# Performance work log

Measured on AMD Instinct MI355X. Metric: run time of the kernel, lower is better.

The kernel has to match this reference:

```python
import jax, jax.numpy as jnp
import numpy as np

B, D_IN, H = 32768, 256, 128
N_TASK, N_EXP, N_SHARE = 2, 4, 4


def setup_inputs() -> dict:
    key = jax.random.key(0)
    ks = jax.random.split(key, 4)
    s = 1.0 / np.sqrt(D_IN)
    return {
        "x": jax.random.normal(ks[0], (B, D_IN), dtype=jnp.float32),
        "W_share": jax.random.normal(ks[1], (N_SHARE, D_IN, H), dtype=jnp.float32) * s,
        "b_share": jnp.zeros((N_SHARE, H), dtype=jnp.float32),
        "W_task": jax.random.normal(ks[2], (N_TASK, N_EXP, D_IN, H), dtype=jnp.float32) * s,
        "b_task": jnp.zeros((N_TASK, N_EXP, H), dtype=jnp.float32),
        "W_gate": jax.random.normal(ks[3], (N_TASK, D_IN, N_SHARE + N_EXP), dtype=jnp.float32) * s,
        "b_gate": jnp.zeros((N_TASK, N_SHARE + N_EXP), dtype=jnp.float32),
    }


def reference(x, W_share, b_share, W_task, b_task, W_gate, b_gate):
    # shared experts: [B, N_SHARE, H]
    share = jax.nn.relu(jnp.einsum('bd,edh->beh', x, W_share) + b_share)
    # task-specific experts: [T, B, N_EXP, H]
    task = jax.nn.relu(jnp.einsum('bd,tedh->tbeh', x, W_task) + b_task[:, None])
    # gates: [T, B, N_SHARE + N_EXP], softmax over experts
    gate = jax.nn.softmax(jnp.einsum('bd,tdg->tbg', x, W_gate) + b_gate[:, None], axis=-1)
    # concat order matches original: share_net first, then task experts
    share_b = jnp.broadcast_to(share[None], (N_TASK, B, N_SHARE, H))
    experts = jnp.concatenate([share_b, task], axis=2)  # [T, B, N_SHARE+N_EXP, H]
    towers = jnp.einsum('tbeh,tbe->tbh', experts, gate)  # [T, B, H]
    return towers
```

## Files before the change

kernel.cpp:

```cpp
#include <hip/hip_runtime.h>


#define ROWSTRIDE 264
#define EXPERT_USHORTS (128 * ROWSTRIDE)
#define EXPERT_BYTES   (EXPERT_USHORTS * 2)
#define WAVE_SHARE     8448
#define WTG_USHORTS    (16 * ROWSTRIDE)

typedef __attribute__((ext_vector_type(8))) short short8;
typedef __attribute__((ext_vector_type(4))) float float4v;

__device__ __forceinline__ unsigned short f2bf(float f) {
  unsigned u = __builtin_bit_cast(unsigned, f);
  u += 0x7FFFu + ((u >> 16) & 1u);
  return (unsigned short)(u >> 16);
}

typedef const __attribute__((address_space(1))) unsigned int gu32;
typedef __attribute__((address_space(3))) unsigned int lu32;

__device__ __forceinline__ void gl_lds16(const void* g, void* l) {
  __builtin_amdgcn_global_load_lds((gu32*)g, (lu32*)l, 16, 0, 0);
}
__device__ __forceinline__ void gl_lds4(const void* g, void* l) {
  __builtin_amdgcn_global_load_lds((gu32*)g, (lu32*)l, 4, 0, 0);
}

__device__ __forceinline__ void stage_expert(const unsigned short* WT, int e,
                                             unsigned short* dst, int w, int lane) {
  const char* g = (const char*)WT + (size_t)e * EXPERT_BYTES + w * WAVE_SHARE;
  char* l = (char*)dst + w * WAVE_SHARE;
  #pragma unroll
  for (int i = 0; i < 8; ++i)
    gl_lds16(g + i * 1024 + lane * 16, l + i * 1024);
  gl_lds4(g + 8192 + lane * 4, l + 8192);
}

__global__ __launch_bounds__(256)
void prep_kernel(const float* __restrict__ Ws,
                 const float* __restrict__ Wt,
                 const float* __restrict__ Wg,
                 unsigned short* __restrict__ WT) {
  int bid = blockIdx.x;
  int tid = threadIdx.x;
  if (bid < 96) {
    __shared__ float tile[64][65];
    int e  = bid >> 3;
    int kt = (bid >> 1) & 3;
    int ht = bid & 1;
    const float* src = (e < 4) ? Ws + ((size_t)e << 15)
                               : Wt + ((size_t)(e - 4) << 15);
    int m = tid & 15, n = tid >> 4;
    #pragma unroll
    for (int i = 0; i < 4; ++i) {
      int kl = i * 16 + n;
      float4 v = *(const float4*)&src[(size_t)(kt * 64 + kl) * 128 + ht * 64 + m * 4];
      tile[kl][m * 4 + 0] = v.x;
      tile[kl][m * 4 + 1] = v.y;
      tile[kl][m * 4 + 2] = v.z;
      tile[kl][m * 4 + 3] = v.w;
    }
    __syncthreads();
    #pragma unroll
    for (int i = 0; i < 4; ++i) {
      int hl = i * 16 + n;
      ushort4 o;
      o.x = f2bf(tile[m * 4 + 0][hl]);
      o.y = f2bf(tile[m * 4 + 1][hl]);
      o.z = f2bf(tile[m * 4 + 2][hl]);
      o.w = f2bf(tile[m * 4 + 3][hl]);
      *(ushort4*)&WT[(size_t)e * EXPERT_USHORTS + (size_t)(ht * 64 + hl) * ROWSTRIDE
                     + kt * 64 + m * 4] = o;
    }
  } else {
    unsigned short* WTg = WT + 12 * EXPERT_USHORTS;
    for (int idx = tid; idx < WTG_USHORTS; idx += 256) {
      int n = idx / ROWSTRIDE, c = idx - n * ROWSTRIDE;
      int t = n >> 3, g = n & 7;
      WTg[idx] = (c < 256) ? f2bf(Wg[(size_t)(t * 256 + c) * 8 + g]) : (unsigned short)0;
    }
    for (int j = tid; j < 12 * 128; j += 256) {
      int e = j >> 7, h = j & 127;
      unsigned short* p = WT + (size_t)e * EXPERT_USHORTS + (size_t)h * ROWSTRIDE + 256;
      #pragma unroll
      for (int q = 0; q < 8; ++q) p[q] = 0;
    }
  }
}

__global__ __launch_bounds__(512, 2)
void dmoe_main(const float* __restrict__ x,
               const unsigned short* __restrict__ WT,
               const float* __restrict__ b_share,
               const float* __restrict__ b_task,
               const float* __restrict__ b_gate,
               float* __restrict__ out) {
  __shared__ unsigned short Bs0[EXPERT_USHORTS];
  __shared__ unsigned short Bs1[EXPERT_USHORTS];
  __shared__ float gatesT[16 * 132];
  __shared__ float biasLds[12 * 128];

  const int tid  = threadIdx.x;
  const int lane = tid & 63;
  const int w    = tid >> 6;
  const int col  = lane & 15;
  const int quad = lane >> 4;
  const int mg   = w >> 2;
  const int ng   = w & 3;
  const int blk  = blockIdx.x;

  {
    const char* wg = (const char*)(WT + 12 * EXPERT_USHORTS);
    gl_lds16(wg + w * 1024 + lane * 16, (char*)Bs1 + w * 1024);
    if (w == 0) gl_lds4(wg + 8192 + lane * 4, (char*)Bs1 + 8192);
  }
  stage_expert(WT, 0, Bs0, w, lane);

  for (int i = tid; i < 1536; i += 512)
    biasLds[i] = (i < 512) ? b_share[i] : b_task[i - 512];

  float bg = b_gate[col];

  short8 A[4][8];
  {
    const float* xb = x + ((size_t)blk * 128 + mg * 64 + col) * 256 + quad * 8;
    #pragma unroll
    for (int mt = 0; mt < 4; ++mt) {
      const float* xr = xb + (size_t)mt * 16 * 256;
      #pragma unroll
      for (int k = 0; k < 8; ++k) {
        float4 u = *(const float4*)(xr + k * 32);
        float4 v = *(const float4*)(xr + k * 32 + 4);
        short8 fr;
        fr[0] = (short)f2bf(u.x); fr[1] = (short)f2bf(u.y);
        fr[2] = (short)f2bf(u.z); fr[3] = (short)f2bf(u.w);
        fr[4] = (short)f2bf(v.x); fr[5] = (short)f2bf(v.y);
        fr[6] = (short)f2bf(v.z); fr[7] = (short)f2bf(v.w);
        A[mt][k] = fr;
      }
    }
  }
  __syncthreads();

  #pragma unroll
  for (int mt = 0; mt < 4; ++mt) {
    float4v ag = {0.f, 0.f, 0.f, 0.f};
    #pragma unroll
    for (int k = 0; k < 8; ++k) {
      short8 bfr = *(const short8*)((const char*)Bs1 + col * 528 + k * 64 + quad * 16);
      ag = __builtin_amdgcn_mfma_f32_16x16x32_bf16(A[mt][k], bfr, ag, 0, 0, 0);
    }
    #pragma unroll
    for (int r = 0; r < 4; ++r) {
      float vlog = ag[r] + bg;
      float m = vlog;
      m = fmaxf(m, __shfl_xor(m, 1));
      m = fmaxf(m, __shfl_xor(m, 2));
      m = fmaxf(m, __shfl_xor(m, 4));
      float p = __expf(vlog - m);
      float s = p;
      s += __shfl_xor(s, 1);
      s += __shfl_xor(s, 2);
      s += __shfl_xor(s, 4);
      if (ng == 0)
        gatesT[col * 132 + mg * 64 + mt * 16 + quad * 4 + r] = p / s;
    }
  }
  __syncthreads();
  stage_expert(WT, 1, Bs1, w, lane);

  float tw[2][4][2][4];
  #pragma unroll
  for (int t = 0; t < 2; ++t)
    #pragma unroll
    for (int mt = 0; mt < 4; ++mt)
      #pragma unroll
      for (int nt = 0; nt < 2; ++nt)
        #pragma unroll
        for (int r = 0; r < 4; ++r)
          tw[t][mt][nt][r] = 0.f;

  const int hbase = ng * 32;

  #pragma unroll 1
  for (int ep = 0; ep < 6; ++ep) {
    #pragma unroll
    for (int half = 0; half < 2; ++half) {
      const int e = 2 * ep + half;
      const unsigned short* Bb = half ? Bs1 : Bs0;
      float b0 = biasLds[e * 128 + hbase + col];
      float b1 = biasLds[e * 128 + hbase + 16 + col];
      #pragma unroll
      for (int nt = 0; nt < 2; ++nt) {
        const char* bbase = (const char*)Bb + (hbase + nt * 16 + col) * 528 + quad * 16;
        float4v acc[4];
        #pragma unroll
        for (int mt = 0; mt < 4; ++mt) acc[mt] = (float4v){0.f, 0.f, 0.f, 0.f};
        #pragma unroll
        for (int k = 0; k < 8; ++k) {
          short8 bfr = *(const short8*)(bbase + k * 64);
          acc[0] = __builtin_amdgcn_mfma_f32_16x16x32_bf16(A[0][k], bfr, acc[0], 0, 0, 0);
          acc[1] = __builtin_amdgcn_mfma_f32_16x16x32_bf16(A[1][k], bfr, acc[1], 0, 0, 0);
          acc[2] = __builtin_amdgcn_mfma_f32_16x16x32_bf16(A[2][k], bfr, acc[2], 0, 0, 0);
          acc[3] = __builtin_amdgcn_mfma_f32_16x16x32_bf16(A[3][k], bfr, acc[3], 0, 0, 0);
        }
        float bb = nt ? b1 : b0;
        if (e < 4) {
          #pragma unroll
          for (int mt = 0; mt < 4; ++mt) {
            int rb = mg * 64 + mt * 16 + quad * 4;
            float4 g0 = *(const float4*)&gatesT[e * 132 + rb];
            float4 g1 = *(const float4*)&gatesT[(8 + e) * 132 + rb];
            #pragma unroll
            for (int r = 0; r < 4; ++r) {
              float v = fmaxf(acc[mt][r] + bb, 0.f);
              tw[0][mt][nt][r] += ((const float*)&g0)[r] * v;
              tw[1][mt][nt][r] += ((const float*)&g1)[r] * v;
            }
          }
        } else {
          const int t  = (e >= 8);
          const int gc = t ? e + 4 : e;
          #pragma unroll
          for (int mt = 0; mt < 4; ++mt) {
            int rb = mg * 64 + mt * 16 + quad * 4;
            float4 g = *(const float4*)&gatesT[gc * 132 + rb];
            #pragma unroll
            for (int r = 0; r < 4; ++r) {
              float v = fmaxf(acc[mt][r] + bb, 0.f);
              tw[t][mt][nt][r] += ((const float*)&g)[r] * v;
            }
          }
        }
      }
      __syncthreads();
      if (e + 2 < 12) {
        if (half == 0) stage_expert(WT, e + 2, Bs0, w, lane);
        else           stage_expert(WT, e + 2, Bs1, w, lane);
      }
    }
  }

  #pragma unroll
  for (int t = 0; t < 2; ++t)
    #pragma unroll
    for (int mt = 0; mt < 4; ++mt)
      #pragma unroll
      for (int r = 0; r < 4; ++r) {
        size_t row = (size_t)blk * 128 + mg * 64 + mt * 16 + quad * 4 + r;
        float* op = out + ((size_t)t << 22) + row * 128 + hbase;
        op[col]      = tw[t][mt][0][r];
        op[16 + col] = tw[t][mt][1][r];
      }
}

extern "C" void kernel_launch(void* const* d_in, const int* in_sizes, int n_in,
                              void* d_out, int out_size, void* d_ws, size_t ws_size,
                              hipStream_t stream) {
  const float* x       = (const float*)d_in[0];
  const float* W_share = (const float*)d_in[1];
  const float* b_share = (const float*)d_in[2];
  const float* W_task  = (const float*)d_in[3];
  const float* b_task  = (const float*)d_in[4];
  const float* W_gate  = (const float*)d_in[5];
  const float* b_gate  = (const float*)d_in[6];
  float* out = (float*)d_out;
  unsigned short* WT = (unsigned short*)d_ws;

  prep_kernel<<<97, 256, 0, stream>>>(W_share, W_task, W_gate, WT);
  dmoe_main<<<256, 512, 0, stream>>>(x, WT, b_share, b_task, b_gate, out);
}
```

Baseline: 177.9 us.

## Split blocks per task with k-quarter weight staging through registers

The main kernel now launches 1024 blocks of 256 threads, each handling 64 rows for a single task (8 experts), where before each block covered 128 rows for both tasks. Weights are re-laid out in k-quarter units with a 72-element row stride and are double-buffered through registers into LDS instead of direct global-to-LDS loads. A per-block rotation of the expert order spreads weight reads across L2. This aims to raise occupancy and cut LDS footprint, but the shared experts' GEMMs are now computed twice (once per task), adding matmul work, and each step adds more barriers.

```diff
diff --git a/kernel.cpp b/kernel.cpp
--- a/kernel.cpp
+++ b/kernel.cpp
@@ -1,14 +1,13 @@
 #include <hip/hip_runtime.h>
 
-
-#define ROWSTRIDE 264
-#define EXPERT_USHORTS (128 * ROWSTRIDE)
-#define EXPERT_BYTES   (EXPERT_USHORTS * 2)
-#define WAVE_SHARE     8448
-#define WTG_USHORTS    (16 * ROWSTRIDE)
 
 typedef __attribute__((ext_vector_type(8))) short short8;
 typedef __attribute__((ext_vector_type(4))) float float4v;
+
+#define UNIT_B   18432
+#define ROW_B    144
+#define WAVE_B   4608
+#define WGT_OFF  442368
 
 __device__ __forceinline__ unsigned short f2bf(float f) {
   unsigned u = __builtin_bit_cast(unsigned, f);
@@ -16,31 +15,15 @@
   return (unsigned short)(u >> 16);
 }
 
-typedef const __attribute__((address_space(1))) unsigned int gu32;
-typedef __attribute__((address_space(3))) unsigned int lu32;
-
-__device__ __forceinline__ void gl_lds16(const void* g, void* l) {
-  __builtin_amdgcn_global_load_lds((gu32*)g, (lu32*)l, 16, 0, 0);
-}
-__device__ __forceinline__ void gl_lds4(const void* g, void* l) {
-  __builtin_amdgcn_global_load_lds((gu32*)g, (lu32*)l, 4, 0, 0);
-}
-
-__device__ __forceinline__ void stage_expert(const unsigned short* WT, int e,
-                                             unsigned short* dst, int w, int lane) {
-  const char* g = (const char*)WT + (size_t)e * EXPERT_BYTES + w * WAVE_SHARE;
-  char* l = (char*)dst + w * WAVE_SHARE;
-  #pragma unroll
-  for (int i = 0; i < 8; ++i)
-    gl_lds16(g + i * 1024 + lane * 16, l + i * 1024);
-  gl_lds4(g + 8192 + lane * 4, l + 8192);
+__device__ __forceinline__ int slot2e(int sr, int t) {
+  return (sr < 4) ? sr : 4 + t * 4 + (sr - 4);
 }
 
 __global__ __launch_bounds__(256)
 void prep_kernel(const float* __restrict__ Ws,
                  const float* __restrict__ Wt,
                  const float* __restrict__ Wg,
-                 unsigned short* __restrict__ WT) {
+                 unsigned short* __restrict__ WT2) {
   int bid = blockIdx.x;
   int tid = threadIdx.x;
   if (bid < 96) {
@@ -64,68 +47,73 @@
     #pragma unroll
     for (int i = 0; i < 4; ++i) {
       int hl = i * 16 + n;
+      size_t base = ((size_t)(e * 4 + kt) * 128 + ht * 64 + hl) * 72;
       ushort4 o;
       o.x = f2bf(tile[m * 4 + 0][hl]);
       o.y = f2bf(tile[m * 4 + 1][hl]);
       o.z = f2bf(tile[m * 4 + 2][hl]);
       o.w = f2bf(tile[m * 4 + 3][hl]);
-      *(ushort4*)&WT[(size_t)e * EXPERT_USHORTS + (size_t)(ht * 64 + hl) * ROWSTRIDE
-                     + kt * 64 + m * 4] = o;
+      *(ushort4*)&WT2[base + m * 4] = o;
+      if (m < 2) {
+        ushort4 z = {0, 0, 0, 0};
+        *(ushort4*)&WT2[base + 64 + m * 4] = z;
+      }
     }
   } else {
-    unsigned short* WTg = WT + 12 * EXPERT_USHORTS;
-    for (int idx = tid; idx < WTG_USHORTS; idx += 256) {
-      int n = idx / ROWSTRIDE, c = idx - n * ROWSTRIDE;
+    unsigned short* WgT = WT2 + WGT_OFF;
+    #pragma unroll
+    for (int it = 0; it < 16; ++it) {
+      int j = it * 256 + tid;
+      int n = j >> 8, k = j & 255;
       int t = n >> 3, g = n & 7;
-      WTg[idx] = (c < 256) ? f2bf(Wg[(size_t)(t * 256 + c) * 8 + g]) : (unsigned short)0;
-    }
-    for (int j = tid; j < 12 * 128; j += 256) {
-      int e = j >> 7, h = j & 127;
-      unsigned short* p = WT + (size_t)e * EXPERT_USHORTS + (size_t)h * ROWSTRIDE + 256;
-      #pragma unroll
-      for (int q = 0; q < 8; ++q) p[q] = 0;
-    }
-  }
-}
-
-__global__ __launch_bounds__(512, 2)
+      WgT[j] = f2bf(Wg[(size_t)(t * 256 + k) * 8 + g]);
+    }
+  }
+}
+
+__global__ __launch_bounds__(256, 3)
 void dmoe_main(const float* __restrict__ x,
-               const unsigned short* __restrict__ WT,
+               const unsigned short* __restrict__ WT2,
                const float* __restrict__ b_share,
                const float* __restrict__ b_task,
                const float* __restrict__ b_gate,
                float* __restrict__ out) {
-  __shared__ unsigned short Bs0[EXPERT_USHORTS];
-  __shared__ unsigned short Bs1[EXPERT_USHORTS];
-  __shared__ float gatesT[16 * 132];
-  __shared__ float biasLds[12 * 128];
+  __shared__ unsigned short Bs0[UNIT_B / 2];
+  __shared__ unsigned short Bs1[UNIT_B / 2];
+  __shared__ float gates[8 * 68];
 
   const int tid  = threadIdx.x;
   const int lane = tid & 63;
   const int w    = tid >> 6;
   const int col  = lane & 15;
   const int quad = lane >> 4;
-  const int mg   = w >> 2;
-  const int ng   = w & 3;
+  const int mg   = w & 1;
+  const int ng   = w >> 1;
   const int blk  = blockIdx.x;
-
-  {
-    const char* wg = (const char*)(WT + 12 * EXPERT_USHORTS);
-    gl_lds16(wg + w * 1024 + lane * 16, (char*)Bs1 + w * 1024);
-    if (w == 0) gl_lds4(wg + 8192 + lane * 4, (char*)Bs1 + 8192);
-  }
-  stage_expert(WT, 0, Bs0, w, lane);
-
-  for (int i = tid; i < 1536; i += 512)
-    biasLds[i] = (i < 512) ? b_share[i] : b_task[i - 512];
-
-  float bg = b_gate[col];
-
-  short8 A[4][8];
-  {
-    const float* xb = x + ((size_t)blk * 128 + mg * 64 + col) * 256 + quad * 8;
-    #pragma unroll
-    for (int mt = 0; mt < 4; ++mt) {
+  const int t    = blk & 1;
+  const int rt   = blk >> 1;
+  const int rot  = (blk >> 3) & 7;
+  const int hb   = ng * 64;
+
+  const char* WT2b = (const char*)WT2;
+
+  const int sr0 = rot;
+  const int e0  = slot2e(sr0, t);
+  uint4 p0, p1, p2, p3; uint2 p4;
+  {
+    const char* g = WT2b + (size_t)(e0 * 4 + 0) * UNIT_B + w * WAVE_B;
+    p0 = *(const uint4*)(g + lane * 16);
+    p1 = *(const uint4*)(g + 1024 + lane * 16);
+    p2 = *(const uint4*)(g + 2048 + lane * 16);
+    p3 = *(const uint4*)(g + 3072 + lane * 16);
+    p4 = *(const uint2*)(g + 4096 + lane * 8);
+  }
+
+  short8 A[2][8];
+  {
+    const float* xb = x + ((size_t)rt * 64 + mg * 32 + col) * 256 + quad * 8;
+    #pragma unroll
+    for (int mt = 0; mt < 2; ++mt) {
       const float* xr = xb + (size_t)mt * 16 * 256;
       #pragma unroll
       for (int k = 0; k < 8; ++k) {
@@ -140,118 +128,142 @@
       }
     }
   }
+
+  {
+    const unsigned short* WgT = WT2 + WGT_OFF;
+    int gr = (col < 8) ? col : 7;
+    const unsigned short* bp = WgT + (size_t)(t * 8 + gr) * 256 + quad * 8;
+    short8 Bg[8];
+    #pragma unroll
+    for (int k = 0; k < 8; ++k) Bg[k] = *(const short8*)(bp + k * 32);
+    float bg = b_gate[t * 8 + gr];
+    #pragma unroll
+    for (int mt = 0; mt < 2; ++mt) {
+      float4v ag = {0.f, 0.f, 0.f, 0.f};
+      #pragma unroll
+      for (int k = 0; k < 8; ++k)
+        ag = __builtin_amdgcn_mfma_f32_16x16x32_bf16(A[mt][k], Bg[k], ag, 0, 0, 0);
+      #pragma unroll
+      for (int r = 0; r < 4; ++r) {
+        float vlog = ag[r] + bg;
+        float m = vlog;
+        m = fmaxf(m, __shfl_xor(m, 1));
+        m = fmaxf(m, __shfl_xor(m, 2));
+        m = fmaxf(m, __shfl_xor(m, 4));
+        float p = __expf(vlog - m);
+        float s = p;
+        s += __shfl_xor(s, 1);
+        s += __shfl_xor(s, 2);
+        s += __shfl_xor(s, 4);
+        if (ng == 0 && col < 8)
+          gates[col * 68 + mg * 32 + mt * 16 + quad * 4 + r] = p / s;
+      }
+    }
+  }
+
+  {
+    char* l = (char*)Bs0 + w * WAVE_B;
+    *(uint4*)(l + lane * 16)        = p0;
+    *(uint4*)(l + 1024 + lane * 16) = p1;
+    *(uint4*)(l + 2048 + lane * 16) = p2;
+    *(uint4*)(l + 3072 + lane * 16) = p3;
+    *(uint2*)(l + 4096 + lane * 8)  = p4;
+  }
   __syncthreads();
 
+  float tw[2][4][4];
   #pragma unroll
-  for (int mt = 0; mt < 4; ++mt) {
-    float4v ag = {0.f, 0.f, 0.f, 0.f};
-    #pragma unroll
-    for (int k = 0; k < 8; ++k) {
-      short8 bfr = *(const short8*)((const char*)Bs1 + col * 528 + k * 64 + quad * 16);
-      ag = __builtin_amdgcn_mfma_f32_16x16x32_bf16(A[mt][k], bfr, ag, 0, 0, 0);
-    }
-    #pragma unroll
-    for (int r = 0; r < 4; ++r) {
-      float vlog = ag[r] + bg;
-      float m = vlog;
-      m = fmaxf(m, __shfl_xor(m, 1));
-      m = fmaxf(m, __shfl_xor(m, 2));
-      m = fmaxf(m, __shfl_xor(m, 4));
-      float p = __expf(vlog - m);
-      float s = p;
-      s += __shfl_xor(s, 1);
-      s += __shfl_xor(s, 2);
-      s += __shfl_xor(s, 4);
-      if (ng == 0)
-        gatesT[col * 132 + mg * 64 + mt * 16 + quad * 4 + r] = p / s;
-    }
-  }
-  __syncthreads();
-  stage_expert(WT, 1, Bs1, w, lane);
-
-  float tw[2][4][2][4];
-  #pragma unroll
-  for (int t = 0; t < 2; ++t)
-    #pragma unroll
-    for (int mt = 0; mt < 4; ++mt)
-      #pragma unroll
-      for (int nt = 0; nt < 2; ++nt)
+  for (int mt = 0; mt < 2; ++mt)
+    #pragma unroll
+    for (int nt = 0; nt < 4; ++nt)
+      #pragma unroll
+      for (int r = 0; r < 4; ++r)
+        tw[mt][nt][r] = 0.f;
+
+  #pragma unroll 1
+  for (int s = 0; s < 8; ++s) {
+    const int sr  = (s + rot) & 7;
+    const int e   = slot2e(sr, t);
+    const int gc  = sr;
+    const int sr2 = (s + 1 + rot) & 7;
+    const int e2  = slot2e(sr2, t);
+    const float* bp = (sr < 4) ? (b_share + sr * 128)
+                               : (b_task + (size_t)(t * 4 + (sr - 4)) * 128);
+    float bias[4];
+    #pragma unroll
+    for (int nt = 0; nt < 4; ++nt) bias[nt] = bp[hb + nt * 16 + col];
+
+    float4v acc[2][4];
+    #pragma unroll
+    for (int mt = 0; mt < 2; ++mt)
+      #pragma unroll
+      for (int nt = 0; nt < 4; ++nt)
+        acc[mt][nt] = (float4v){0.f, 0.f, 0.f, 0.f};
+
+    #pragma unroll
+    for (int kq = 0; kq < 4; ++kq) {
+      const bool doStage = !(s == 7 && kq == 3);
+      const int  en  = (kq < 3) ? e : e2;
+      const int  kqn = (kq + 1) & 3;
+      uint4 q0, q1, q2, q3; uint2 q4;
+      if (doStage) {
+        const char* g = WT2b + (size_t)(en * 4 + kqn) * UNIT_B + w * WAVE_B;
+        q0 = *(const uint4*)(g + lane * 16);
+        q1 = *(const uint4*)(g + 1024 + lane * 16);
+        q2 = *(const uint4*)(g + 2048 + lane * 16);
+        q3 = *(const uint4*)(g + 3072 + lane * 16);
+        q4 = *(const uint2*)(g + 4096 + lane * 8);
+      }
+      {
+        const char* Bb = (const char*)((kq & 1) ? Bs1 : Bs0);
         #pragma unroll
-        for (int r = 0; r < 4; ++r)
-          tw[t][mt][nt][r] = 0.f;
-
-  const int hbase = ng * 32;
-
-  #pragma unroll 1
-  for (int ep = 0; ep < 6; ++ep) {
-    #pragma unroll
-    for (int half = 0; half < 2; ++half) {
-      const int e = 2 * ep + half;
-      const unsigned short* Bb = half ? Bs1 : Bs0;
-      float b0 = biasLds[e * 128 + hbase + col];
-      float b1 = biasLds[e * 128 + hbase + 16 + col];
-      #pragma unroll
-      for (int nt = 0; nt < 2; ++nt) {
-        const char* bbase = (const char*)Bb + (hbase + nt * 16 + col) * 528 + quad * 16;
-        float4v acc[4];
+        for (int kk = 0; kk < 2; ++kk) {
+          #pragma unroll
+          for (int nt = 0; nt < 4; ++nt) {
+            short8 bfr = *(const short8*)(Bb + (hb + nt * 16 + col) * ROW_B
+                                          + kk * 64 + quad * 16);
+            acc[0][nt] = __builtin_amdgcn_mfma_f32_16x16x32_bf16(
+                A[0][kq * 2 + kk], bfr, acc[0][nt], 0, 0, 0);
+            acc[1][nt] = __builtin_amdgcn_mfma_f32_16x16x32_bf16(
+                A[1][kq * 2 + kk], bfr, acc[1][nt], 0, 0, 0);
+          }
+        }
+      }
+      if (doStage) {
+        char* l = (char*)((kq & 1) ? Bs0 : Bs1) + w * WAVE_B;
+        *(uint4*)(l + lane * 16)        = q0;
+        *(uint4*)(l + 1024 + lane * 16) = q1;
+        *(uint4*)(l + 2048 + lane * 16) = q2;
+        *(uint4*)(l + 3072 + lane * 16) = q3;
+        *(uint2*)(l + 4096 + lane * 8)  = q4;
+      }
+      if (kq == 3) {
         #pragma unroll
-        for (int mt = 0; mt < 4; ++mt) acc[mt] = (float4v){0.f, 0.f, 0.f, 0.f};
-        #pragma unroll
-        for (int k = 0; k < 8; ++k) {
-          short8 bfr = *(const short8*)(bbase + k * 64);
-          acc[0] = __builtin_amdgcn_mfma_f32_16x16x32_bf16(A[0][k], bfr, acc[0], 0, 0, 0);
-          acc[1] = __builtin_amdgcn_mfma_f32_16x16x32_bf16(A[1][k], bfr, acc[1], 0, 0, 0);
-          acc[2] = __builtin_amdgcn_mfma_f32_16x16x32_bf16(A[2][k], bfr, acc[2], 0, 0, 0);
-          acc[3] = __builtin_amdgcn_mfma_f32_16x16x32_bf16(A[3][k], bfr, acc[3], 0, 0, 0);
-        }
-        float bb = nt ? b1 : b0;
-        if (e < 4) {
+        for (int mt = 0; mt < 2; ++mt) {
+          float4 gv = *(const float4*)&gates[gc * 68 + mg * 32 + mt * 16 + quad * 4];
           #pragma unroll
-          for (int mt = 0; mt < 4; ++mt) {
-            int rb = mg * 64 + mt * 16 + quad * 4;
-            float4 g0 = *(const float4*)&gatesT[e * 132 + rb];
-            float4 g1 = *(const float4*)&gatesT[(8 + e) * 132 + rb];
+          for (int nt = 0; nt < 4; ++nt)
             #pragma unroll
             for (int r = 0; r < 4; ++r) {
-              float v = fmaxf(acc[mt][r] + bb, 0.f);
-              tw[0][mt][nt][r] += ((const float*)&g0)[r] * v;
-              tw[1][mt][nt][r] += ((const float*)&g1)[r] * v;
+              float v = fmaxf(acc[mt][nt][r] + bias[nt], 0.f);
+              tw[mt][nt][r] += ((const float*)&gv)[r] * v;
             }
-          }
-        } else {
-          const int t  = (e >= 8);
-          const int gc = t ? e + 4 : e;
-          #pragma unroll
-          for (int mt = 0; mt < 4; ++mt) {
-            int rb = mg * 64 + mt * 16 + quad * 4;
-            float4 g = *(const float4*)&gatesT[gc * 132 + rb];
-            #pragma unroll
-            for (int r = 0; r < 4; ++r) {
-              float v = fmaxf(acc[mt][r] + bb, 0.f);
-              tw[t][mt][nt][r] += ((const float*)&g)[r] * v;
-            }
-          }
         }
       }
       __syncthreads();
-      if (e + 2 < 12) {
-        if (half == 0) stage_expert(WT, e + 2, Bs0, w, lane);
-        else           stage_expert(WT, e + 2, Bs1, w, lane);
-      }
     }
   }
 
   #pragma unroll
-  for (int t = 0; t < 2; ++t)
-    #pragma unroll
-    for (int mt = 0; mt < 4; ++mt)
-      #pragma unroll
-      for (int r = 0; r < 4; ++r) {
-        size_t row = (size_t)blk * 128 + mg * 64 + mt * 16 + quad * 4 + r;
-        float* op = out + ((size_t)t << 22) + row * 128 + hbase;
-        op[col]      = tw[t][mt][0][r];
-        op[16 + col] = tw[t][mt][1][r];
-      }
+  for (int mt = 0; mt < 2; ++mt)
+    #pragma unroll
+    for (int r = 0; r < 4; ++r) {
+      size_t row = (size_t)rt * 64 + mg * 32 + mt * 16 + quad * 4 + r;
+      float* op = out + ((size_t)t << 22) + row * 128 + hb;
+      #pragma unroll
+      for (int nt = 0; nt < 4; ++nt)
+        op[nt * 16 + col] = tw[mt][nt][r];
+    }
 }
 
 extern "C" void kernel_launch(void* const* d_in, const int* in_sizes, int n_in,
@@ -265,8 +277,8 @@
   const float* W_gate  = (const float*)d_in[5];
   const float* b_gate  = (const float*)d_in[6];
   float* out = (float*)d_out;
-  unsigned short* WT = (unsigned short*)d_ws;
-
-  prep_kernel<<<97, 256, 0, stream>>>(W_share, W_task, W_gate, WT);
-  dmoe_main<<<256, 512, 0, stream>>>(x, WT, b_share, b_task, b_gate, out);
-}
+  unsigned short* WT2 = (unsigned short*)d_ws;
+
+  prep_kernel<<<97, 256, 0, stream>>>(W_share, W_task, W_gate, WT2);
+  dmoe_main<<<1024, 256, 0, stream>>>(x, WT2, b_share, b_task, b_gate, out);
+}
```

Result: faster. 171.5 us (-3.6%).
